# Kernel tuning notes

Hardware: AMD Instinct MI355X
Metric: run time of the kernel (lower is better)

Reference implementation:

```python
import jax, jax.numpy as jnp
import numpy as np

IN_F = 128
OUT_F = 64


def _xavier(key, shape, gain=1.414):
    fan_in, fan_out = shape[0], shape[1]
    bound = gain * np.sqrt(6.0 / (fan_in + fan_out))
    return jax.random.uniform(key, shape, jnp.float32, -bound, bound)


def setup_inputs() -> dict:
    key = jax.random.key(0)
    ks = jax.random.split(key, 11)
    features = jax.random.normal(ks[0], (2, 32, 2048, IN_F), dtype=jnp.float32)
    d = {"features": features}
    for i in range(4):
        d[f"W{i+1}"] = _xavier(ks[1 + 2 * i], (IN_F, 2 * OUT_F))
        d[f"a{i+1}"] = _xavier(ks[2 + 2 * i], (2 * OUT_F, 1))
    d["Wo"] = _xavier(ks[9], (8 * OUT_F, OUT_F))
    return d


def _head(features, W, a):
    # features: [b,g,n,i]; W: [i,j]; a: [j,1]
    Wx = jnp.einsum('bgni,ij->bgnj', features, W)          # [b,g,n,2F]
    att = jax.nn.softmax(Wx @ a, axis=2)                   # softmax over nodes, [b,g,n,1]
    return jnp.einsum('bgno,bgnj->bgj', att, Wx)           # pooled [b,g,2F]


def reference(features, W1, a1, W2, a2, W3, a3, W4, a4, Wo):
    h1 = _head(features, W1, a1)
    h2 = _head(features, W2, a2)
    h3 = _head(features, W3, a3)
    h4 = _head(features, W4, a4)
    multi = jnp.concatenate([h1, h2, h3, h4], axis=2)      # [b,g,8F]
    return jax.nn.elu(multi @ Wo)                          # [b,g,F]
```

## Files before the change

kernel.cpp:

```cpp
#include <hip/hip_runtime.h>
#include <math.h>

#define BG     64
#define NN     2048
#define F      128
#define OUTF   64
#define NSLICE 16

#define OFF_WEFF 0
#define OFF_FP   512
#define OFF_LP   (512 + BG * NSLICE * 4 * F)

__global__ __launch_bounds__(512) void k_weff(
    const float* __restrict__ W1, const float* __restrict__ a1,
    const float* __restrict__ W2, const float* __restrict__ a2,
    const float* __restrict__ W3, const float* __restrict__ a3,
    const float* __restrict__ W4, const float* __restrict__ a4,
    float* __restrict__ ws) {
  int t = threadIdx.x;
  int h = t >> 7, i = t & 127;
  const float* W = (h == 0) ? W1 : (h == 1) ? W2 : (h == 2) ? W3 : W4;
  const float* a = (h == 0) ? a1 : (h == 1) ? a2 : (h == 2) ? a3 : a4;
  float acc = 0.f;
#pragma unroll 16
  for (int j = 0; j < F; ++j) acc += W[i * F + j] * a[j];
  ws[OFF_WEFF + h * F + i] = acc;
}

__global__ __launch_bounds__(256) void k_main(
    const float* __restrict__ feat, float* __restrict__ ws) {
  int g = blockIdx.x >> 4;
  int slice = blockIdx.x & (NSLICE - 1);
  int t = threadIdx.x;
  int lane = t & 31;
  int hw = t >> 5;

  const float* weff = ws + OFF_WEFF;
  float4 w4[4];
#pragma unroll
  for (int h = 0; h < 4; ++h) w4[h] = ((const float4*)(weff + h * F))[lane];

  const float* fbase = feat + ((size_t)g * NN + slice * (NN / NSLICE)) * F;

  float4 acc[4];
#pragma unroll
  for (int h = 0; h < 4; ++h) acc[h] = make_float4(0.f, 0.f, 0.f, 0.f);
  float se[4] = {0.f, 0.f, 0.f, 0.f};

#pragma unroll 4
  for (int it = 0; it < (NN / NSLICE) / 8; ++it) {
    int n = it * 8 + hw;
    float4 f = ((const float4*)(fbase + (size_t)n * F))[lane];
    float p[4];
#pragma unroll
    for (int h = 0; h < 4; ++h)
      p[h] = f.x * w4[h].x + f.y * w4[h].y + f.z * w4[h].z + f.w * w4[h].w;
#pragma unroll
    for (int off = 16; off; off >>= 1) {
#pragma unroll
      for (int h = 0; h < 4; ++h) p[h] += __shfl_xor(p[h], off);
    }
#pragma unroll
    for (int h = 0; h < 4; ++h) {
      float e = __expf(p[h]);
      se[h] += e;
      acc[h].x += e * f.x; acc[h].y += e * f.y;
      acc[h].z += e * f.z; acc[h].w += e * f.w;
    }
  }

  __shared__ float4 part[8][4][32];
  __shared__ float sume[8][4];
#pragma unroll
  for (int h = 0; h < 4; ++h) part[hw][h][lane] = acc[h];
  if (lane == 0) {
#pragma unroll
    for (int h = 0; h < 4; ++h) sume[hw][h] = se[h];
  }
  __syncthreads();

  if (t < 128) {
    int h = t >> 5, l = t & 31;
    float4 s = part[0][h][l];
#pragma unroll
    for (int q = 1; q < 8; ++q) {
      float4 o = part[q][h][l];
      s.x += o.x; s.y += o.y; s.z += o.z; s.w += o.w;
    }
    ((float4*)(ws + OFF_FP + ((size_t)(g * NSLICE + slice) * 4 + h) * F))[l] = s;
  }
  if (t < 4) {
    float s = 0.f;
#pragma unroll
    for (int q = 0; q < 8; ++q) s += sume[q][t];
    ws[OFF_LP + (g * NSLICE + slice) * 4 + t] = s;
  }
}

__global__ __launch_bounds__(512) void k_final(
    const float* __restrict__ W1, const float* __restrict__ W2,
    const float* __restrict__ W3, const float* __restrict__ W4,
    const float* __restrict__ Wo, const float* __restrict__ ws,
    float* __restrict__ out) {
  int g = blockIdx.x;
  int t = threadIdx.x;
  __shared__ float fp[512];
  __shared__ float multi[512];
  __shared__ float invl[4];
  __shared__ float part[8][64];

  if (t < 4) {
    float s = 0.f;
#pragma unroll
    for (int sl = 0; sl < NSLICE; ++sl)
      s += ws[OFF_LP + (g * NSLICE + sl) * 4 + t];
    invl[t] = 1.0f / s;
  }
  float s = 0.f;
  const float* fpb = ws + OFF_FP + (size_t)g * NSLICE * 512 + t;
#pragma unroll
  for (int sl = 0; sl < NSLICE; ++sl) s += fpb[sl * 512];
  __syncthreads();
  fp[t] = s * invl[t >> 7];
  __syncthreads();

  int h = t >> 7, col = t & 127;
  const float* W = (h == 0) ? W1 : (h == 1) ? W2 : (h == 2) ? W3 : W4;
  const float* fph = fp + h * F;
  float acc = 0.f;
#pragma unroll 16
  for (int i = 0; i < F; ++i) acc += fph[i] * W[i * F + col];
  multi[t] = acc;
  __syncthreads();

  int o = t & 63, chunk = t >> 6;
  const float* mk = multi + chunk * 64;
  const float* wk = Wo + (size_t)chunk * 64 * OUTF + o;
  float p = 0.f;
#pragma unroll 16
  for (int k = 0; k < 64; ++k) p += mk[k] * wk[k * OUTF];
  part[chunk][o] = p;
  __syncthreads();

  if (t < 64) {
    float acc2 = 0.f;
#pragma unroll
    for (int c = 0; c < 8; ++c) acc2 += part[c][t];
    out[g * OUTF + t] = (acc2 > 0.f) ? acc2 : expm1f(acc2);
  }
}

extern "C" void kernel_launch(void* const* d_in, const int* in_sizes, int n_in,
                              void* d_out, int out_size, void* d_ws, size_t ws_size,
                              hipStream_t stream) {
  const float* feat = (const float*)d_in[0];
  const float* W1 = (const float*)d_in[1];
  const float* a1 = (const float*)d_in[2];
  const float* W2 = (const float*)d_in[3];
  const float* a2 = (const float*)d_in[4];
  const float* W3 = (const float*)d_in[5];
  const float* a3 = (const float*)d_in[6];
  const float* W4 = (const float*)d_in[7];
  const float* a4 = (const float*)d_in[8];
  const float* Wo = (const float*)d_in[9];
  float* ws = (float*)d_ws;
  float* out = (float*)d_out;

  k_weff<<<1, 512, 0, stream>>>(W1, a1, W2, a2, W3, a3, W4, a4, ws);
  k_main<<<BG * NSLICE, 256, 0, stream>>>(feat, ws);
  k_final<<<BG, 512, 0, stream>>>(W1, W2, W3, W4, Wo, ws, out);
}
```

Baseline: 133.4 us.

## Fuse three kernels into one with last-block reduction and shuffle-packed head dots

Merges the weight-folding, main pooling and final projection kernels into a single launch. Every block recomputes the folded W·a vectors into shared memory, and the last block per graph, found with an atomic counter, performs the final reduction, projection and ELU. The per-head dot-product reduction is also restructured so four heads share one butterfly and one exp per lane, cutting shuffles and exp calls. The cost is redundant W·a work in all 1024 blocks (64K FMAs each), an extra memset launch, and a serialized tail done by 256 threads instead of 512.

```diff
diff --git a/kernel.cpp b/kernel.cpp
--- a/kernel.cpp
+++ b/kernel.cpp
@@ -7,76 +7,91 @@
 #define OUTF   64
 #define NSLICE 16
 
-#define OFF_WEFF 0
-#define OFF_FP   512
-#define OFF_LP   (512 + BG * NSLICE * 4 * F)
-
-__global__ __launch_bounds__(512) void k_weff(
+#define OFF_FP   0
+#define OFF_LP   (BG * NSLICE * 4 * F)
+#define OFF_CNT  (OFF_LP + BG * NSLICE * 4)
+
+__global__ __launch_bounds__(256) void k_fused(
+    const float* __restrict__ feat,
     const float* __restrict__ W1, const float* __restrict__ a1,
     const float* __restrict__ W2, const float* __restrict__ a2,
     const float* __restrict__ W3, const float* __restrict__ a3,
     const float* __restrict__ W4, const float* __restrict__ a4,
-    float* __restrict__ ws) {
-  int t = threadIdx.x;
-  int h = t >> 7, i = t & 127;
-  const float* W = (h == 0) ? W1 : (h == 1) ? W2 : (h == 2) ? W3 : W4;
-  const float* a = (h == 0) ? a1 : (h == 1) ? a2 : (h == 2) ? a3 : a4;
-  float acc = 0.f;
-#pragma unroll 16
-  for (int j = 0; j < F; ++j) acc += W[i * F + j] * a[j];
-  ws[OFF_WEFF + h * F + i] = acc;
-}
-
-__global__ __launch_bounds__(256) void k_main(
-    const float* __restrict__ feat, float* __restrict__ ws) {
+    const float* __restrict__ Wo,
+    float* __restrict__ ws, float* __restrict__ out) {
   int g = blockIdx.x >> 4;
   int slice = blockIdx.x & (NSLICE - 1);
   int t = threadIdx.x;
   int lane = t & 31;
   int hw = t >> 5;
 
-  const float* weff = ws + OFF_WEFF;
+  __shared__ float weff[4][F];
+  __shared__ float4 part[8][4][32];
+  __shared__ float sume[8][4];
+  __shared__ int isLast;
+  __shared__ float fpL[512];
+  __shared__ float multi[512];
+  __shared__ float invl[4];
+  __shared__ float fpart[4][64];
+
+  {
+    int idx = t;
+#pragma unroll
+    for (int r = 0; r < 2; ++r, idx += 256) {
+      int h = idx >> 7, i = idx & 127;
+      const float* W = (h == 0) ? W1 : (h == 1) ? W2 : (h == 2) ? W3 : W4;
+      const float* a = (h == 0) ? a1 : (h == 1) ? a2 : (h == 2) ? a3 : a4;
+      float acc = 0.f;
+#pragma unroll 16
+      for (int j = 0; j < F; ++j) acc += W[i * F + j] * a[j];
+      weff[h][i] = acc;
+    }
+  }
+  __syncthreads();
+
   float4 w4[4];
 #pragma unroll
-  for (int h = 0; h < 4; ++h) w4[h] = ((const float4*)(weff + h * F))[lane];
+  for (int h = 0; h < 4; ++h) w4[h] = ((const float4*)weff[h])[lane];
 
   const float* fbase = feat + ((size_t)g * NN + slice * (NN / NSLICE)) * F;
-
   float4 acc[4];
 #pragma unroll
-  for (int h = 0; h < 4; ++h) acc[h] = make_float4(0.f, 0.f, 0.f, 0.f);
-  float se[4] = {0.f, 0.f, 0.f, 0.f};
+  for (int k = 0; k < 4; ++k) acc[k] = make_float4(0.f, 0.f, 0.f, 0.f);
+  float se0 = 0.f;
+  int l1 = lane & 1, l2 = lane & 2;
 
 #pragma unroll 4
   for (int it = 0; it < (NN / NSLICE) / 8; ++it) {
     int n = it * 8 + hw;
     float4 f = ((const float4*)(fbase + (size_t)n * F))[lane];
-    float p[4];
-#pragma unroll
-    for (int h = 0; h < 4; ++h)
-      p[h] = f.x * w4[h].x + f.y * w4[h].y + f.z * w4[h].z + f.w * w4[h].w;
-#pragma unroll
-    for (int off = 16; off; off >>= 1) {
-#pragma unroll
-      for (int h = 0; h < 4; ++h) p[h] += __shfl_xor(p[h], off);
-    }
-#pragma unroll
-    for (int h = 0; h < 4; ++h) {
-      float e = __expf(p[h]);
-      se[h] += e;
-      acc[h].x += e * f.x; acc[h].y += e * f.y;
-      acc[h].z += e * f.z; acc[h].w += e * f.w;
-    }
-  }
-
-  __shared__ float4 part[8][4][32];
-  __shared__ float sume[8][4];
-#pragma unroll
-  for (int h = 0; h < 4; ++h) part[hw][h][lane] = acc[h];
-  if (lane == 0) {
-#pragma unroll
-    for (int h = 0; h < 4; ++h) sume[hw][h] = se[h];
-  }
+    float p0 = f.x * w4[0].x + f.y * w4[0].y + f.z * w4[0].z + f.w * w4[0].w;
+    float p1 = f.x * w4[1].x + f.y * w4[1].y + f.z * w4[1].z + f.w * w4[1].w;
+    float p2 = f.x * w4[2].x + f.y * w4[2].y + f.z * w4[2].z + f.w * w4[2].w;
+    float p3 = f.x * w4[3].x + f.y * w4[3].y + f.z * w4[3].z + f.w * w4[3].w;
+    float a01 = l1 ? p1 : p0, b01 = l1 ? p0 : p1;
+    a01 += __shfl_xor(b01, 1);
+    float a23 = l1 ? p3 : p2, b23 = l1 ? p2 : p3;
+    a23 += __shfl_xor(b23, 1);
+    float c = l2 ? a23 : a01, d = l2 ? a01 : a23;
+    c += __shfl_xor(d, 2);
+    c += __shfl_xor(c, 4);
+    c += __shfl_xor(c, 8);
+    c += __shfl_xor(c, 16);
+    float e0 = __expf(c);
+    float e1 = __shfl_xor(e0, 1);
+    float e2 = __shfl_xor(e0, 2);
+    float e3 = __shfl_xor(e0, 3);
+    se0 += e0;
+    acc[0].x += e0 * f.x; acc[0].y += e0 * f.y; acc[0].z += e0 * f.z; acc[0].w += e0 * f.w;
+    acc[1].x += e1 * f.x; acc[1].y += e1 * f.y; acc[1].z += e1 * f.z; acc[1].w += e1 * f.w;
+    acc[2].x += e2 * f.x; acc[2].y += e2 * f.y; acc[2].z += e2 * f.z; acc[2].w += e2 * f.w;
+    acc[3].x += e3 * f.x; acc[3].y += e3 * f.y; acc[3].z += e3 * f.z; acc[3].w += e3 * f.w;
+  }
+
+  int hbase = lane & 3;
+#pragma unroll
+  for (int k = 0; k < 4; ++k) part[hw][hbase ^ k][lane] = acc[k];
+  if (lane < 4) sume[hw][lane] = se0;
   __syncthreads();
 
   if (t < 128) {
@@ -95,19 +110,18 @@
     for (int q = 0; q < 8; ++q) s += sume[q][t];
     ws[OFF_LP + (g * NSLICE + slice) * 4 + t] = s;
   }
-}
-
-__global__ __launch_bounds__(512) void k_final(
-    const float* __restrict__ W1, const float* __restrict__ W2,
-    const float* __restrict__ W3, const float* __restrict__ W4,
-    const float* __restrict__ Wo, const float* __restrict__ ws,
-    float* __restrict__ out) {
-  int g = blockIdx.x;
-  int t = threadIdx.x;
-  __shared__ float fp[512];
-  __shared__ float multi[512];
-  __shared__ float invl[4];
-  __shared__ float part[8][64];
+  __syncthreads();
+
+  if (t == 0) {
+    __threadfence();
+    int* cnt = (int*)(ws + OFF_CNT);
+    int old = atomicAdd(&cnt[g], 1);
+    isLast = (old == NSLICE - 1) ? 1 : 0;
+  }
+  __syncthreads();
+  if (!isLast) return;
+  if (t == 0) __threadfence();
+  __syncthreads();
 
   if (t < 4) {
     float s = 0.f;
@@ -116,37 +130,51 @@
       s += ws[OFF_LP + (g * NSLICE + sl) * 4 + t];
     invl[t] = 1.0f / s;
   }
-  float s = 0.f;
-  const float* fpb = ws + OFF_FP + (size_t)g * NSLICE * 512 + t;
-#pragma unroll
-  for (int sl = 0; sl < NSLICE; ++sl) s += fpb[sl * 512];
-  __syncthreads();
-  fp[t] = s * invl[t >> 7];
-  __syncthreads();
-
-  int h = t >> 7, col = t & 127;
-  const float* W = (h == 0) ? W1 : (h == 1) ? W2 : (h == 2) ? W3 : W4;
-  const float* fph = fp + h * F;
-  float acc = 0.f;
+  float sums[2];
+#pragma unroll
+  for (int r = 0; r < 2; ++r) {
+    int idx = t + r * 256;
+    const float* fpb = ws + OFF_FP + (size_t)g * NSLICE * 512 + idx;
+    float s = 0.f;
+#pragma unroll
+    for (int sl = 0; sl < NSLICE; ++sl) s += fpb[sl * 512];
+    sums[r] = s;
+  }
+  __syncthreads();
+#pragma unroll
+  for (int r = 0; r < 2; ++r) {
+    int idx = t + r * 256;
+    fpL[idx] = sums[r] * invl[idx >> 7];
+  }
+  __syncthreads();
+
+#pragma unroll
+  for (int r = 0; r < 2; ++r) {
+    int idx = t + r * 256;
+    int h = idx >> 7, col = idx & 127;
+    const float* W = (h == 0) ? W1 : (h == 1) ? W2 : (h == 2) ? W3 : W4;
+    const float* fph = fpL + h * F;
+    float acc2 = 0.f;
 #pragma unroll 16
-  for (int i = 0; i < F; ++i) acc += fph[i] * W[i * F + col];
-  multi[t] = acc;
-  __syncthreads();
-
-  int o = t & 63, chunk = t >> 6;
-  const float* mk = multi + chunk * 64;
-  const float* wk = Wo + (size_t)chunk * 64 * OUTF + o;
-  float p = 0.f;
+    for (int i = 0; i < F; ++i) acc2 += fph[i] * W[i * F + col];
+    multi[idx] = acc2;
+  }
+  __syncthreads();
+
+  {
+    int o = t & 63, chunk = t >> 6;
+    const float* mk = multi + chunk * 128;
+    const float* wk = Wo + (size_t)chunk * 128 * OUTF + o;
+    float p = 0.f;
 #pragma unroll 16
-  for (int k = 0; k < 64; ++k) p += mk[k] * wk[k * OUTF];
-  part[chunk][o] = p;
+    for (int k = 0; k < 128; ++k) p += mk[k] * wk[k * OUTF];
+    fpart[chunk][o] = p;
+  }
   __syncthreads();
 
   if (t < 64) {
-    float acc2 = 0.f;
-#pragma unroll
-    for (int c = 0; c < 8; ++c) acc2 += part[c][t];
-    out[g * OUTF + t] = (acc2 > 0.f) ? acc2 : expm1f(acc2);
+    float s = fpart[0][t] + fpart[1][t] + fpart[2][t] + fpart[3][t];
+    out[g * OUTF + t] = (s > 0.f) ? s : expm1f(s);
   }
 }
 
@@ -166,7 +194,9 @@
   float* ws = (float*)d_ws;
   float* out = (float*)d_out;
 
-  k_weff<<<1, 512, 0, stream>>>(W1, a1, W2, a2, W3, a3, W4, a4, ws);
-  k_main<<<BG * NSLICE, 256, 0, stream>>>(feat, ws);
-  k_final<<<BG, 512, 0, stream>>>(W1, W2, W3, W4, Wo, ws, out);
+  hipMemsetAsync((char*)d_ws + OFF_CNT * sizeof(float), 0,
+                 BG * sizeof(int), stream);
+
+  k_fused<<<BG * NSLICE, 256, 0, stream>>>(feat, W1, a1, W2, a2, W3, a3,
+                                           W4, a4, Wo, ws, out);
 }
```

Measured after the change: 190.3 us. +42.6%, slower.

## Stage node tile in LDS and split scoring from weighted pooling

Applied to the files above, without the earlier changes.

k_main now loads its whole 128-node x 128-feature slice into a 64 KB shared-memory tile with an XOR swizzle, issuing 16 float4 loads per thread up front. One thread per node computes the four head scores from LDS, with no cross-lane shuffle reduction. A second pass over the tile accumulates the exp-weighted features. This is meant to expose more memory-level parallelism and remove the shuffle chains. In exchange, only 128 of 256 threads compute, occupancy falls because of the large LDS use, and there are extra barriers.

```diff
diff --git a/kernel.cpp b/kernel.cpp
--- a/kernel.cpp
+++ b/kernel.cpp
@@ -32,68 +32,83 @@
   int g = blockIdx.x >> 4;
   int slice = blockIdx.x & (NSLICE - 1);
   int t = threadIdx.x;
-  int lane = t & 31;
-  int hw = t >> 5;
 
-  const float* weff = ws + OFF_WEFF;
-  float4 w4[4];
+  __shared__ float4 sfeat[128 * 32];
+  __shared__ float4 weffL[4 * 32];
+  __shared__ float4 eL[128];
+  __shared__ float4 pacc[4][4][32];
+  __shared__ float4 sePart[4];
+
+  if (t < 128) weffL[t] = ((const float4*)(ws + OFF_WEFF))[t];
+
+  const float4* fb =
+      (const float4*)(feat + ((size_t)g * NN + slice * 128) * F);
+  float4 ld[16];
 #pragma unroll
-  for (int h = 0; h < 4; ++h) w4[h] = ((const float4*)(weff + h * F))[lane];
-
-  const float* fbase = feat + ((size_t)g * NN + slice * (NN / NSLICE)) * F;
-
-  float4 acc[4];
+  for (int k = 0; k < 16; ++k) ld[k] = fb[k * 256 + t];
 #pragma unroll
-  for (int h = 0; h < 4; ++h) acc[h] = make_float4(0.f, 0.f, 0.f, 0.f);
-  float se[4] = {0.f, 0.f, 0.f, 0.f};
-
-#pragma unroll 4
-  for (int it = 0; it < (NN / NSLICE) / 8; ++it) {
-    int n = it * 8 + hw;
-    float4 f = ((const float4*)(fbase + (size_t)n * F))[lane];
-    float p[4];
-#pragma unroll
-    for (int h = 0; h < 4; ++h)
-      p[h] = f.x * w4[h].x + f.y * w4[h].y + f.z * w4[h].z + f.w * w4[h].w;
-#pragma unroll
-    for (int off = 16; off; off >>= 1) {
-#pragma unroll
-      for (int h = 0; h < 4; ++h) p[h] += __shfl_xor(p[h], off);
-    }
-#pragma unroll
-    for (int h = 0; h < 4; ++h) {
-      float e = __expf(p[h]);
-      se[h] += e;
-      acc[h].x += e * f.x; acc[h].y += e * f.y;
-      acc[h].z += e * f.z; acc[h].w += e * f.w;
-    }
-  }
-
-  __shared__ float4 part[8][4][32];
-  __shared__ float sume[8][4];
-#pragma unroll
-  for (int h = 0; h < 4; ++h) part[hw][h][lane] = acc[h];
-  if (lane == 0) {
-#pragma unroll
-    for (int h = 0; h < 4; ++h) sume[hw][h] = se[h];
+  for (int k = 0; k < 16; ++k) {
+    int j = k * 256 + t;
+    int n = j >> 5, c = j & 31;
+    sfeat[n * 32 + (c ^ (n & 31))] = ld[k];
   }
   __syncthreads();
 
   if (t < 128) {
-    int h = t >> 5, l = t & 31;
-    float4 s = part[0][h][l];
-#pragma unroll
-    for (int q = 1; q < 8; ++q) {
-      float4 o = part[q][h][l];
-      s.x += o.x; s.y += o.y; s.z += o.z; s.w += o.w;
+    int n = t, sw = n & 31, base = n * 32;
+    float p0 = 0.f, p1 = 0.f, p2 = 0.f, p3 = 0.f;
+#pragma unroll 8
+    for (int c = 0; c < 32; ++c) {
+      float4 f = sfeat[base + (c ^ sw)];
+      float4 w0 = weffL[c], w1 = weffL[32 + c], w2 = weffL[64 + c],
+             w3 = weffL[96 + c];
+      p0 += f.x * w0.x + f.y * w0.y + f.z * w0.z + f.w * w0.w;
+      p1 += f.x * w1.x + f.y * w1.y + f.z * w1.z + f.w * w1.w;
+      p2 += f.x * w2.x + f.y * w2.y + f.z * w2.z + f.w * w2.w;
+      p3 += f.x * w3.x + f.y * w3.y + f.z * w3.z + f.w * w3.w;
     }
-    ((float4*)(ws + OFF_FP + ((size_t)(g * NSLICE + slice) * 4 + h) * F))[l] = s;
+    eL[n] = make_float4(__expf(p0), __expf(p1), __expf(p2), __expf(p3));
   }
-  if (t < 4) {
-    float s = 0.f;
-#pragma unroll
-    for (int q = 0; q < 8; ++q) s += sume[q][t];
-    ws[OFF_LP + (g * NSLICE + slice) * 4 + t] = s;
+  __syncthreads();
+
+  if (t < 128) {
+    int i4 = t & 31, q = t >> 5;
+    float4 a0 = make_float4(0.f, 0.f, 0.f, 0.f), a1 = a0, a2 = a0, a3 = a0;
+    float4 se = a0;
+#pragma unroll 8
+    for (int nn = 0; nn < 32; ++nn) {
+      int n = q * 32 + nn;
+      float4 f = sfeat[n * 32 + (i4 ^ (n & 31))];
+      float4 e = eL[n];
+      a0.x += e.x * f.x; a0.y += e.x * f.y; a0.z += e.x * f.z; a0.w += e.x * f.w;
+      a1.x += e.y * f.x; a1.y += e.y * f.y; a1.z += e.y * f.z; a1.w += e.y * f.w;
+      a2.x += e.z * f.x; a2.y += e.z * f.y; a2.z += e.z * f.z; a2.w += e.z * f.w;
+      a3.x += e.w * f.x; a3.y += e.w * f.y; a3.z += e.w * f.z; a3.w += e.w * f.w;
+      se.x += e.x; se.y += e.y; se.z += e.z; se.w += e.w;
+    }
+    pacc[0][q][i4] = a0; pacc[1][q][i4] = a1;
+    pacc[2][q][i4] = a2; pacc[3][q][i4] = a3;
+    if (i4 == 0) sePart[q] = se;
+  }
+  __syncthreads();
+
+  if (t < 128) {
+    int i4 = t & 31, h = t >> 5;
+    float4 s0 = pacc[h][0][i4], s1 = pacc[h][1][i4];
+    float4 s2 = pacc[h][2][i4], s3 = pacc[h][3][i4];
+    float4 s = make_float4(s0.x + s1.x + s2.x + s3.x,
+                           s0.y + s1.y + s2.y + s3.y,
+                           s0.z + s1.z + s2.z + s3.z,
+                           s0.w + s1.w + s2.w + s3.w);
+    ((float4*)(ws + OFF_FP))[(size_t)(g * NSLICE + slice) * 128 + h * 32 + i4] = s;
+  }
+  if (t == 0) {
+    float4 L = make_float4(
+        sePart[0].x + sePart[1].x + sePart[2].x + sePart[3].x,
+        sePart[0].y + sePart[1].y + sePart[2].y + sePart[3].y,
+        sePart[0].z + sePart[1].z + sePart[2].z + sePart[3].z,
+        sePart[0].w + sePart[1].w + sePart[2].w + sePart[3].w);
+    ((float4*)(ws + OFF_LP))[g * NSLICE + slice] = L;
   }
 }
 
```

Result: no change. 133.3 us (-0.1%).
